# Kernel tuning notes

Measured on AMD Instinct MI355X. Metric: run time of the kernel, lower is better.

## Reference

```python
import jax, jax.numpy as jnp
import numpy as np

N = 50000      # nodes
E = 800000     # edges (avg degree 16)
F_IN = 32      # raw node feature dim
H = 96         # hidden_channels == encoder.output_dim (skip_connection=True)
EDGE_DIM = 16
L = 3          # num_layers
B = 50         # graphs in batch
MSG_IN = 2 * H + 1 + EDGE_DIM   # [h_i, h_j, ||dpos||^2, edge_attr]
NODE_IN = 2 * H                 # [h_i, aggregated message]


def setup_inputs() -> dict:
    key = jax.random.key(0)
    ks = jax.random.split(key, 14)

    def w(k, shape):
        fan_in = shape[-2]
        return jax.random.normal(k, shape, jnp.float32) * (1.0 / np.sqrt(fan_in))

    return {
        "x": jax.random.normal(ks[0], (N, F_IN), jnp.float32),
        "pos": jax.random.normal(ks[1], (N, 3), jnp.float32),
        "edge_index": jax.random.randint(ks[2], (2, E), 0, N),
        "edge_attr": jax.random.normal(ks[3], (E, EDGE_DIM), jnp.float32),
        "batch_indices": jnp.sort(jax.random.randint(ks[4], (N,), 0, B)),
        # encoder (modeled as a linear projection to H)
        "We": w(ks[5], (F_IN, H)), "be": jnp.zeros((H,), jnp.float32),
        # per-layer EGNN edge MLP: Linear(MSG_IN,H)-SiLU-Linear(H,H)-SiLU
        "eW1": w(ks[6], (L, MSG_IN, H)), "eb1": jnp.zeros((L, H), jnp.float32),
        "eW2": w(ks[7], (L, H, H)), "eb2": jnp.zeros((L, H), jnp.float32),
        # per-layer EGNN node MLP: Linear(NODE_IN,H)-SiLU-Linear(H,H)
        "nW1": w(ks[8], (L, NODE_IN, H)), "nb1": jnp.zeros((L, H), jnp.float32),
        "nW2": w(ks[9], (L, H, H)), "nb2": jnp.zeros((L, H), jnp.float32),
        "Wl": w(ks[10], (H, 1)), "bl": jnp.zeros((1,), jnp.float32),
    }


def reference(x, pos, edge_index, edge_attr, batch_indices,
              We, be, eW1, eb1, eW2, eb2, nW1, nb1, nW2, nb2, Wl, bl):
    silu = jax.nn.silu
    src, dst = edge_index[0], edge_index[1]

    # encoder: project raw features to hidden dim
    h = x @ We + be                                    # [N, H]

    # squared pairwise distances along edges (pos fixed, update_pos=False)
    rel = pos[src] - pos[dst]                          # [E, 3]
    d2 = jnp.sum(rel * rel, axis=-1, keepdims=True)    # [E, 1]

    for l in range(L):
        feat = jnp.concatenate([h[src], h[dst], d2, edge_attr], axis=-1)  # [E, MSG_IN]
        m = silu(silu(feat @ eW1[l] + eb1[l]) @ eW2[l] + eb2[l])          # [E, H]
        agg = jax.ops.segment_sum(m, dst, num_segments=N)                 # [N, H]
        upd = silu(jnp.concatenate([h, agg], axis=-1) @ nW1[l] + nb1[l]) @ nW2[l] + nb2[l]
        h = h + upd  # skip_connection=True

    # global_mean_pool over graphs
    counts = jax.ops.segment_sum(jnp.ones((N, 1), h.dtype), batch_indices, num_segments=B)
    pooled = jax.ops.segment_sum(h, batch_indices, num_segments=B) / jnp.maximum(counts, 1.0)

    return pooled @ Wl + bl                            # [B, 1]
```

## Files before the change

kernel.cpp:

```cpp
#include <hip/hip_runtime.h>

#define Nn 50000
#define Ee 800000
#define FIN 32
#define EDIM 16
#define Bb 50
#define SPX 6250

typedef _Float16 half8 __attribute__((ext_vector_type(8)));
typedef float floatx4 __attribute__((ext_vector_type(4)));

#define OFF_WeT 0
#define WT_LAYER(l) (3072 + (l) * 58368)
#define OFF_W1AB 0
#define OFF_W1C  18432
#define OFF_W2   21504
#define OFF_NW1  30720
#define OFF_NW2  49152
#define WT_TOTAL 178176

__device__ __forceinline__ float silu_f(float x) {
    return __fdividef(x, 1.0f + __expf(-x));
}

__device__ __forceinline__ int lower_bound_i(const int* a, int n, int v) {
    int lo = 0, hi = n;
    while (lo < hi) { int m = (lo + hi) >> 1; if (a[m] < v) lo = m + 1; else hi = m; }
    return lo;
}

__device__ __forceinline__ half8 ldg_h8(const _Float16* p) {
    return *(const half8*)p;
}

__device__ __forceinline__ half8 h8_zero() {
    half8 z;
    #pragma unroll
    for (int j = 0; j < 8; j++) z[j] = (_Float16)0.f;
    return z;
}

__global__ void k_prepw(const float* __restrict__ We, const float* __restrict__ eW1,
                        const float* __restrict__ eW2, const float* __restrict__ nW1,
                        const float* __restrict__ nW2, _Float16* __restrict__ wT) {
    int idx = blockIdx.x * 256 + threadIdx.x;
    if (idx >= WT_TOTAL) return;
    float v;
    if (idx < 3072) {
        int n = idx >> 5, k = idx & 31;
        v = We[k * 96 + n];
    } else {
        int j = idx - 3072;
        int l = j / 58368, r = j % 58368;
        const float* eW1l = eW1 + l * 209 * 96;
        if (r < 18432) {
            int n = r / 96, k = r % 96;
            v = (n < 96) ? eW1l[k * 96 + n] : eW1l[(96 + k) * 96 + (n - 96)];
        } else if (r < 21504) {
            int r2 = r - 18432;
            int n = r2 >> 5, k = r2 & 31;
            v = (k < 16) ? eW1l[(193 + k) * 96 + n]
              : (k == 16) ? eW1l[192 * 96 + n] : 0.f;
        } else if (r < 30720) {
            int r2 = r - 21504;
            int n = r2 / 96, k = r2 % 96;
            v = eW2[l * 9216 + k * 96 + n];
        } else if (r < 49152) {
            int r2 = r - 30720;
            int n = r2 / 192, k = r2 % 192;
            v = nW1[l * 18432 + k * 96 + n];
        } else {
            int r2 = r - 49152;
            int n = r2 / 96, k = r2 % 96;
            v = nW2[l * 9216 + k * 96 + n];
        }
    }
    wT[idx] = (_Float16)v;
}

__global__ void k_prep(const int* __restrict__ ei, int* __restrict__ counts) {
    int e = blockIdx.x * 256 + threadIdx.x;
    if (e >= Ee) return;
    atomicAdd(&counts[ei[Ee + e]], 1);
}

__global__ void k_scanA(const int* __restrict__ counts, int* __restrict__ rowstart,
                        int* __restrict__ bsums) {
    __shared__ int s[256];
    int b = blockIdx.x, t = threadIdx.x, i = b * 256 + t;
    int v = (i < Nn) ? counts[i] : 0;
    s[t] = v;
    __syncthreads();
    for (int off = 1; off < 256; off <<= 1) {
        int add = (t >= off) ? s[t - off] : 0;
        __syncthreads();
        s[t] += add;
        __syncthreads();
    }
    if (i < Nn) rowstart[i + 1] = s[t];
    if (t == 255) bsums[b] = s[255];
}

__global__ void k_scanB(int* __restrict__ bsums, int nb) {
    __shared__ int s[256];
    int t = threadIdx.x;
    int v = (t < nb) ? bsums[t] : 0;
    s[t] = v;
    __syncthreads();
    for (int off = 1; off < 256; off <<= 1) {
        int add = (t >= off) ? s[t - off] : 0;
        __syncthreads();
        s[t] += add;
        __syncthreads();
    }
    if (t < nb) bsums[t] = s[t] - v;
}

__global__ void k_scanC(int* __restrict__ rowstart, const int* __restrict__ bsums) {
    int b = blockIdx.x, t = threadIdx.x, i = b * 256 + t;
    if (i < Nn) rowstart[i + 1] += bsums[b];
    if (i == 0 && b == 0) rowstart[0] = 0;
}

__global__ void k_fill(const int* __restrict__ ei, const float* __restrict__ ea,
                       const float* __restrict__ pos, const int* __restrict__ rowstart,
                       int* __restrict__ cur, int* __restrict__ srcs_p,
                       int* __restrict__ dsts_p, _Float16* __restrict__ eap16,
                       _Float16* __restrict__ d2h) {
    int e = blockIdx.x * 256 + threadIdx.x;
    if (e >= Ee) return;
    int s = ei[e], d = ei[Ee + e];
    int slot = rowstart[d] + atomicAdd(&cur[d], 1);
    srcs_p[slot] = s;
    dsts_p[slot] = d;
    float dx = pos[s * 3 + 0] - pos[d * 3 + 0];
    float dy = pos[s * 3 + 1] - pos[d * 3 + 1];
    float dz = pos[s * 3 + 2] - pos[d * 3 + 2];
    float dv = dx * dx + dy * dy + dz * dz;
    const float4* ea4 = (const float4*)ea;
    float4 q0 = ea4[e * 4 + 0], q1 = ea4[e * 4 + 1];
    float4 q2 = ea4[e * 4 + 2], q3 = ea4[e * 4 + 3];
    half8 c0, c1;
    c0[0]=(_Float16)q0.x; c0[1]=(_Float16)q0.y; c0[2]=(_Float16)q0.z; c0[3]=(_Float16)q0.w;
    c0[4]=(_Float16)q1.x; c0[5]=(_Float16)q1.y; c0[6]=(_Float16)q1.z; c0[7]=(_Float16)q1.w;
    c1[0]=(_Float16)q2.x; c1[1]=(_Float16)q2.y; c1[2]=(_Float16)q2.z; c1[3]=(_Float16)q2.w;
    c1[4]=(_Float16)q3.x; c1[5]=(_Float16)q3.y; c1[6]=(_Float16)q3.z; c1[7]=(_Float16)q3.w;
    half8* dst8 = (half8*)(eap16 + (size_t)slot * 16);
    dst8[0] = c0; dst8[1] = c1;
    d2h[slot] = (_Float16)dv;
}

__global__ __launch_bounds__(256, 4)
void k_encab(const float* __restrict__ x, const _Float16* __restrict__ WeT,
             const float* __restrict__ be, const _Float16* __restrict__ W1abT,
             _Float16* __restrict__ h16, _Float16* __restrict__ A16,
             _Float16* __restrict__ B16, float* __restrict__ agg) {
    __shared__ _Float16 x16[64][40];
    __shared__ _Float16 hs[64][104];
    int t = threadIdx.x;
    int n0 = blockIdx.x * 64;
    for (int i = t; i < 64 * 32; i += 256) {
        int nl = i >> 5, k = i & 31;
        int n = n0 + nl;
        x16[nl][k] = (_Float16)((n < Nn) ? x[n * FIN + k] : 0.f);
    }
    __syncthreads();
    int lane = t & 63, quad = lane >> 4, lm = lane & 15, w = t >> 6;
    half8 af = *(const half8*)&x16[w * 16 + lm][quad * 8];
    #pragma unroll
    for (int nt = 0; nt < 6; nt++) {
        int col = nt * 16 + lm;
        float b = be[col];
        floatx4 acc = {b, b, b, b};
        half8 bf = ldg_h8(WeT + col * 32 + quad * 8);
        acc = __builtin_amdgcn_mfma_f32_16x16x32_f16(af, bf, acc, 0, 0, 0);
        #pragma unroll
        for (int r = 0; r < 4; r++)
            hs[w * 16 + quad * 4 + r][col] = (_Float16)acc[r];
    }
    __syncthreads();
    #pragma unroll
    for (int i = 0; i < 3; i++) {
        int ci = t + 256 * i;
        int el = ci / 12, c0 = (ci % 12) * 8;
        int n = n0 + el;
        if (n < Nn) *(half8*)(h16 + n * 96 + c0) = *(half8*)&hs[el][c0];
    }
    for (int i = t; i < 64 * 24; i += 256) {
        int el = i / 24, c = (i % 24) * 4;
        int n = n0 + el;
        if (n < Nn) *(float4*)(agg + n * 96 + c) = make_float4(0.f, 0.f, 0.f, 0.f);
    }
    half8 af3[3];
    #pragma unroll
    for (int kt = 0; kt < 3; kt++)
        af3[kt] = *(const half8*)&hs[w * 16 + lm][kt * 32 + quad * 8];
    #pragma unroll
    for (int nt = 0; nt < 12; nt++) {
        int col = nt * 16 + lm;
        floatx4 acc = {0.f, 0.f, 0.f, 0.f};
        #pragma unroll
        for (int kt = 0; kt < 3; kt++) {
            half8 bf = ldg_h8(W1abT + col * 96 + kt * 32 + quad * 8);
            acc = __builtin_amdgcn_mfma_f32_16x16x32_f16(af3[kt], bf, acc, 0, 0, 0);
        }
        #pragma unroll
        for (int r = 0; r < 4; r++) {
            int n = n0 + w * 16 + quad * 4 + r;
            if (n < Nn) {
                if (col < 96) A16[n * 96 + col] = (_Float16)acc[r];
                else          B16[n * 96 + col - 96] = (_Float16)acc[r];
            }
        }
    }
}

__global__ __launch_bounds__(256, 4)
void k_edge(const _Float16* __restrict__ A16, const _Float16* __restrict__ B16,
            const _Float16* __restrict__ eap16, const _Float16* __restrict__ d2h,
            const int* __restrict__ srcs_p, const int* __restrict__ dsts_p,
            const _Float16* __restrict__ W1cT, const float* __restrict__ eb1l,
            const _Float16* __restrict__ W2T, const float* __restrict__ eb2l,
            float* __restrict__ agg) {
    __shared__ _Float16 u16[64][104];
    __shared__ _Float16 W2f[18 * 64 * 8];
    __shared__ _Float16 W1f[6 * 64 * 8];
    __shared__ int ss_s[4][16], ds_s[4][16];

    int t = threadIdx.x;
    int lane = t & 63, quad = lane >> 4, lm = lane & 15, w = t >> 6;

    for (int f = w; f < 18; f += 4) {
        int nt = f / 3, kt = f % 3;
        half8 v = ldg_h8(W2T + (nt * 16 + lm) * 96 + kt * 32 + quad * 8);
        *(half8*)&W2f[(f * 64 + lane) * 8] = v;
    }
    for (int f = w; f < 6; f += 4) {
        half8 v = ldg_h8(W1cT + (f * 16 + lm) * 32 + quad * 8);
        *(half8*)&W1f[(f * 64 + lane) * 8] = v;
    }
    float eb1v[6], eb2v[6];
    #pragma unroll
    for (int nt = 0; nt < 6; nt++) {
        eb1v[nt] = eb1l[nt * 16 + lm];
        eb2v[nt] = eb2l[nt * 16 + lm];
    }
    __syncthreads();

    int xcd = blockIdx.x & 7, ib = blockIdx.x >> 3;
    int slot = ib * 4 + w;
    for (int s = slot; s < SPX; s += 512) {
        int e0 = (xcd * SPX + s) * 16;
        half8 af1;
        if (quad == 0)      af1 = ldg_h8(eap16 + (size_t)(e0 + lm) * 16);
        else if (quad == 1) af1 = ldg_h8(eap16 + (size_t)(e0 + lm) * 16 + 8);
        else { af1 = h8_zero(); if (quad == 2) af1[0] = d2h[e0 + lm]; }
        if (lane < 16) {
            ss_s[w][lane] = srcs_p[e0 + lane];
            ds_s[w][lane] = dsts_p[e0 + lane];
        }
        #pragma unroll
        for (int nt = 0; nt < 6; nt++) {
            floatx4 acc = {eb1v[nt], eb1v[nt], eb1v[nt], eb1v[nt]};
            half8 bf = *(const half8*)&W1f[(nt * 64 + lane) * 8];
            acc = __builtin_amdgcn_mfma_f32_16x16x32_f16(af1, bf, acc, 0, 0, 0);
            #pragma unroll
            for (int r = 0; r < 4; r++)
                u16[w * 16 + quad * 4 + r][nt * 16 + lm] = (_Float16)acc[r];
        }
        #pragma unroll
        for (int i = 0; i < 3; i++) {
            int ci = lane + 64 * i;
            int el = ci / 12, c0 = (ci % 12) * 8;
            half8 av = ldg_h8(A16 + ss_s[w][el] * 96 + c0);
            half8 bv = ldg_h8(B16 + ds_s[w][el] * 96 + c0);
            half8 pv = *(half8*)&u16[w * 16 + el][c0];
            half8 sum = pv + av + bv;
            half8 res;
            #pragma unroll
            for (int j = 0; j < 8; j++)
                res[j] = (_Float16)silu_f((float)sum[j]);
            *(half8*)&u16[w * 16 + el][c0] = res;
        }
        half8 af2[3];
        #pragma unroll
        for (int kt = 0; kt < 3; kt++)
            af2[kt] = *(const half8*)&u16[w * 16 + lm][kt * 32 + quad * 8];
        #pragma unroll
        for (int nt = 0; nt < 6; nt++) {
            floatx4 acc = {eb2v[nt], eb2v[nt], eb2v[nt], eb2v[nt]};
            #pragma unroll
            for (int kt = 0; kt < 3; kt++) {
                half8 bf = *(const half8*)&W2f[((nt * 3 + kt) * 64 + lane) * 8];
                acc = __builtin_amdgcn_mfma_f32_16x16x32_f16(af2[kt], bf, acc, 0, 0, 0);
            }
            #pragma unroll
            for (int r = 0; r < 4; r++)
                u16[w * 16 + quad * 4 + r][nt * 16 + lm] = (_Float16)silu_f(acc[r]);
        }
        if (lane < 48) {
            int c = lane * 2;
            float run0 = 0.f, run1 = 0.f;
            int cd = ds_s[w][0];
            #pragma unroll
            for (int e = 0; e < 16; e++) {
                int dn = ds_s[w][e];
                if (dn != cd) {
                    atomicAdd(&agg[cd * 96 + c], run0);
                    atomicAdd(&agg[cd * 96 + c + 1], run1);
                    run0 = 0.f; run1 = 0.f; cd = dn;
                }
                _Float16 v0 = u16[w * 16 + e][c];
                _Float16 v1 = u16[w * 16 + e][c + 1];
                run0 += (float)v0;
                run1 += (float)v1;
            }
            atomicAdd(&agg[cd * 96 + c], run0);
            atomicAdd(&agg[cd * 96 + c + 1], run1);
        }
    }
}

__global__ __launch_bounds__(256, 4)
void k_nodeab(_Float16* __restrict__ h16, float* __restrict__ agg,
              const _Float16* __restrict__ nW1T, const float* __restrict__ nb1l,
              const _Float16* __restrict__ nW2T, const float* __restrict__ nb2l,
              const _Float16* __restrict__ W1abT, _Float16* __restrict__ A16,
              _Float16* __restrict__ B16, int do_ab) {
    __shared__ _Float16 in16[64][200];
    __shared__ _Float16 t116[64][104];
    int t = threadIdx.x, n0 = blockIdx.x * 64;
    #pragma unroll
    for (int i = 0; i < 3; i++) {
        int ci = t + 256 * i;
        int el = ci / 12, c0 = (ci % 12) * 8;
        int n = n0 + el;
        half8 hv = h8_zero();
        half8 av = h8_zero();
        if (n < Nn) {
            hv = ldg_h8(h16 + n * 96 + c0);
            float4 a = *(const float4*)(agg + n * 96 + c0);
            float4 b = *(const float4*)(agg + n * 96 + c0 + 4);
            av[0]=(_Float16)a.x; av[1]=(_Float16)a.y; av[2]=(_Float16)a.z; av[3]=(_Float16)a.w;
            av[4]=(_Float16)b.x; av[5]=(_Float16)b.y; av[6]=(_Float16)b.z; av[7]=(_Float16)b.w;
        }
        *(half8*)&in16[el][c0] = hv;
        *(half8*)&in16[el][96 + c0] = av;
    }
    __syncthreads();
    int lane = t & 63, quad = lane >> 4, lm = lane & 15, w = t >> 6;
    half8 af[6];
    #pragma unroll
    for (int kt = 0; kt < 6; kt++)
        af[kt] = *(const half8*)&in16[w * 16 + lm][kt * 32 + quad * 8];
    #pragma unroll
    for (int nt = 0; nt < 6; nt++) {
        int col = nt * 16 + lm;
        float b = nb1l[col];
        floatx4 acc = {b, b, b, b};
        #pragma unroll
        for (int kt = 0; kt < 6; kt++) {
            half8 bf = ldg_h8(nW1T + col * 192 + kt * 32 + quad * 8);
            acc = __builtin_amdgcn_mfma_f32_16x16x32_f16(af[kt], bf, acc, 0, 0, 0);
        }
        #pragma unroll
        for (int r = 0; r < 4; r++)
            t116[w * 16 + quad * 4 + r][col] = (_Float16)silu_f(acc[r]);
    }
    half8 af2[3];
    #pragma unroll
    for (int kt = 0; kt < 3; kt++)
        af2[kt] = *(const half8*)&t116[w * 16 + lm][kt * 32 + quad * 8];
    #pragma unroll
    for (int nt = 0; nt < 6; nt++) {
        int col = nt * 16 + lm;
        float b = nb2l[col];
        floatx4 acc = {b, b, b, b};
        #pragma unroll
        for (int kt = 0; kt < 3; kt++) {
            half8 bf = ldg_h8(nW2T + col * 96 + kt * 32 + quad * 8);
            acc = __builtin_amdgcn_mfma_f32_16x16x32_f16(af2[kt], bf, acc, 0, 0, 0);
        }
        #pragma unroll
        for (int r = 0; r < 4; r++) {
            int row = w * 16 + quad * 4 + r;
            float hnew = (float)in16[row][col] + acc[r];
            in16[row][col] = (_Float16)hnew;
        }
    }
    __syncthreads();
    #pragma unroll
    for (int i = 0; i < 3; i++) {
        int ci = t + 256 * i;
        int el = ci / 12, c0 = (ci % 12) * 8;
        int n = n0 + el;
        if (n < Nn) *(half8*)(h16 + n * 96 + c0) = *(half8*)&in16[el][c0];
    }
    if (!do_ab) return;
    half8 af3[3];
    #pragma unroll
    for (int kt = 0; kt < 3; kt++)
        af3[kt] = *(const half8*)&in16[w * 16 + lm][kt * 32 + quad * 8];
    #pragma unroll
    for (int nt = 0; nt < 12; nt++) {
        int col = nt * 16 + lm;
        floatx4 acc = {0.f, 0.f, 0.f, 0.f};
        #pragma unroll
        for (int kt = 0; kt < 3; kt++) {
            half8 bf = ldg_h8(W1abT + col * 96 + kt * 32 + quad * 8);
            acc = __builtin_amdgcn_mfma_f32_16x16x32_f16(af3[kt], bf, acc, 0, 0, 0);
        }
        #pragma unroll
        for (int r = 0; r < 4; r++) {
            int n = n0 + w * 16 + quad * 4 + r;
            if (n < Nn) {
                if (col < 96) A16[n * 96 + col] = (_Float16)acc[r];
                else          B16[n * 96 + col - 96] = (_Float16)acc[r];
            }
        }
    }
    for (int i = t; i < 64 * 24; i += 256) {
        int el = i / 24, c = (i % 24) * 4;
        int n = n0 + el;
        if (n < Nn) *(float4*)(agg + n * 96 + c) = make_float4(0.f, 0.f, 0.f, 0.f);
    }
}

__global__ void k_pool_partial(const _Float16* __restrict__ h16, const int* __restrict__ batch,
                               float* __restrict__ pooled) {
    int g = blockIdx.x >> 2, q = blockIdx.x & 3;
    int start = lower_bound_i(batch, Nn, g);
    int end   = lower_bound_i(batch, Nn, g + 1);
    int len = end - start;
    int chunk = (len + 3) >> 2;
    int s = start + q * chunk;
    int e = min(s + chunk, end);
    int t = threadIdx.x;
    int j = t % 96, r = t / 96;
    float sum = 0.f;
    for (int n = s + r; n < e; n += 2) sum += (float)h16[n * 96 + j];
    atomicAdd(&pooled[g * 96 + j], sum);
}

__global__ void k_final(const float* __restrict__ pooled, const int* __restrict__ batch,
                        const float* __restrict__ Wl, const float* __restrict__ bl,
                        float* __restrict__ out) {
    int g = blockIdx.x, lane = threadIdx.x;
    int start = lower_bound_i(batch, Nn, g);
    int end   = lower_bound_i(batch, Nn, g + 1);
    int cnt = end - start; if (cnt < 1) cnt = 1;
    float v = 0.f;
    for (int j = lane; j < 96; j += 64) v += pooled[g * 96 + j] * Wl[j];
    #pragma unroll
    for (int off = 32; off > 0; off >>= 1) v += __shfl_down(v, off);
    if (lane == 0) out[g] = v / (float)cnt + bl[0];
}

extern "C" void kernel_launch(void* const* d_in, const int* in_sizes, int n_in,
                              void* d_out, int out_size, void* d_ws, size_t ws_size,
                              hipStream_t stream) {
    const float* x     = (const float*)d_in[0];
    const float* pos   = (const float*)d_in[1];
    const int*   ei    = (const int*)d_in[2];
    const float* ea    = (const float*)d_in[3];
    const int*   batch = (const int*)d_in[4];
    const float* We    = (const float*)d_in[5];
    const float* be    = (const float*)d_in[6];
    const float* eW1   = (const float*)d_in[7];
    const float* eb1   = (const float*)d_in[8];
    const float* eW2   = (const float*)d_in[9];
    const float* eb2   = (const float*)d_in[10];
    const float* nW1   = (const float*)d_in[11];
    const float* nb1   = (const float*)d_in[12];
    const float* nW2   = (const float*)d_in[13];
    const float* nb2   = (const float*)d_in[14];
    const float* Wl    = (const float*)d_in[15];
    const float* bl    = (const float*)d_in[16];
    float* out = (float*)d_out;

    float* ws = (float*)d_ws;
    _Float16* h16    = (_Float16*)(ws);
    _Float16* A16    = (_Float16*)(ws + 2400000);
    _Float16* B16    = (_Float16*)(ws + 4800000);
    float*    agg    = ws + 7200000;
    float*    pooled = ws + 12000000;
    int*      counts   = (int*)(ws + 12004800);
    int*      cur      = (int*)(ws + 12054800);
    int*      rowstart = (int*)(ws + 12104800);
    int*      bsums    = (int*)(ws + 12154816);
    int*      srcs_p   = (int*)(ws + 12155072);
    int*      dsts_p   = (int*)(ws + 12955072);
    _Float16* eap16    = (_Float16*)(ws + 13755072);
    _Float16* d2h      = (_Float16*)(ws + 20155072);
    _Float16* wT       = (_Float16*)(ws + 20555072);

    hipMemsetAsync(counts, 0, 2 * 50000 * sizeof(int), stream);
    hipMemsetAsync(pooled, 0, Bb * 96 * sizeof(float), stream);

    k_prepw<<<dim3(696), dim3(256), 0, stream>>>(We, eW1, eW2, nW1, nW2, wT);
    k_prep<<<dim3(3125), dim3(256), 0, stream>>>(ei, counts);
    k_scanA<<<dim3(196), dim3(256), 0, stream>>>(counts, rowstart, bsums);
    k_scanB<<<dim3(1), dim3(256), 0, stream>>>(bsums, 196);
    k_scanC<<<dim3(196), dim3(256), 0, stream>>>(rowstart, bsums);
    k_fill<<<dim3(3125), dim3(256), 0, stream>>>(ei, ea, pos, rowstart, cur,
                                                 srcs_p, dsts_p, eap16, d2h);
    k_encab<<<dim3(782), dim3(256), 0, stream>>>(x, wT + OFF_WeT, be,
        wT + WT_LAYER(0) + OFF_W1AB, h16, A16, B16, agg);

    for (int l = 0; l < 3; l++) {
        const _Float16* wl = wT + WT_LAYER(l);
        k_edge<<<dim3(1024), dim3(256), 0, stream>>>(A16, B16, eap16, d2h,
            srcs_p, dsts_p, wl + OFF_W1C, eb1 + l * 96, wl + OFF_W2, eb2 + l * 96, agg);
        const _Float16* wnext = wT + WT_LAYER(l < 2 ? l + 1 : 0);
        k_nodeab<<<dim3(782), dim3(256), 0, stream>>>(h16, agg,
            wl + OFF_NW1, nb1 + l * 96, wl + OFF_NW2, nb2 + l * 96,
            wnext + OFF_W1AB, A16, B16, (l < 2) ? 1 : 0);
    }
    k_pool_partial<<<dim3(200), dim3(192), 0, stream>>>(h16, batch, pooled);
    k_final<<<dim3(50), dim3(64), 0, stream>>>(pooled, batch, Wl, bl, out);
}
```

Measured before the change: 761.4 us.

## Fuse mean-pool into last node kernel and widen edge scatter to per-column lanes

In the last layer the node-update kernel now sums its 64 updated rows per graph straight from shared memory and adds them atomically into pooled. This removes the separate pooling kernel, the final h16 store and its re-read. The edge kernel's segmented scatter now gives each lane a single column (96 lanes in two passes) instead of column pairs on 48 lanes. That spreads the atomics over more lanes but adds a second pass per wave. The fused pool issues up to a few atomics per block per column into a small pooled array shared by 782 blocks, which may contend.

New measurement: 738.5 us. 1.03x faster.

```diff
diff --git a/kernel.cpp b/kernel.cpp
--- a/kernel.cpp
+++ b/kernel.cpp
@@ -298,25 +298,20 @@
             for (int r = 0; r < 4; r++)
                 u16[w * 16 + quad * 4 + r][nt * 16 + lm] = (_Float16)silu_f(acc[r]);
         }
-        if (lane < 48) {
-            int c = lane * 2;
-            float run0 = 0.f, run1 = 0.f;
-            int cd = ds_s[w][0];
-            #pragma unroll
-            for (int e = 0; e < 16; e++) {
-                int dn = ds_s[w][e];
-                if (dn != cd) {
-                    atomicAdd(&agg[cd * 96 + c], run0);
-                    atomicAdd(&agg[cd * 96 + c + 1], run1);
-                    run0 = 0.f; run1 = 0.f; cd = dn;
+        #pragma unroll
+        for (int p = 0; p < 2; p++) {
+            int c = lane + p * 64;
+            if (c < 96) {
+                float run = 0.f;
+                int cd = ds_s[w][0];
+                #pragma unroll
+                for (int e = 0; e < 16; e++) {
+                    int dn = ds_s[w][e];
+                    if (dn != cd) { atomicAdd(&agg[cd * 96 + c], run); run = 0.f; cd = dn; }
+                    run += (float)u16[w * 16 + e][c];
                 }
-                _Float16 v0 = u16[w * 16 + e][c];
-                _Float16 v1 = u16[w * 16 + e][c + 1];
-                run0 += (float)v0;
-                run1 += (float)v1;
+                atomicAdd(&agg[cd * 96 + c], run);
             }
-            atomicAdd(&agg[cd * 96 + c], run0);
-            atomicAdd(&agg[cd * 96 + c + 1], run1);
         }
     }
 }
@@ -326,9 +321,11 @@
               const _Float16* __restrict__ nW1T, const float* __restrict__ nb1l,
               const _Float16* __restrict__ nW2T, const float* __restrict__ nb2l,
               const _Float16* __restrict__ W1abT, _Float16* __restrict__ A16,
-              _Float16* __restrict__ B16, int do_ab) {
+              _Float16* __restrict__ B16, const int* __restrict__ batch,
+              float* __restrict__ pooled, int do_ab) {
     __shared__ _Float16 in16[64][200];
     __shared__ _Float16 t116[64][104];
+    __shared__ int gb_s[64];
     int t = threadIdx.x, n0 = blockIdx.x * 64;
     #pragma unroll
     for (int i = 0; i < 3; i++) {
@@ -347,6 +344,10 @@
         *(half8*)&in16[el][c0] = hv;
         *(half8*)&in16[el][96 + c0] = av;
     }
+    if (!do_ab && t < 64) {
+        int n = n0 + t;
+        gb_s[t] = (n < Nn) ? batch[n] : -1;
+    }
     __syncthreads();
     int lane = t & 63, quad = lane >> 4, lm = lane & 15, w = t >> 6;
     half8 af[6];
@@ -389,6 +390,22 @@
         }
     }
     __syncthreads();
+    if (!do_ab) {
+        if (t < 96) {
+            float run = 0.f;
+            int cd = gb_s[0];
+            for (int e = 0; e < 64; e++) {
+                int g = gb_s[e];
+                if (g != cd) {
+                    if (cd >= 0) atomicAdd(&pooled[cd * 96 + t], run);
+                    run = 0.f; cd = g;
+                }
+                run += (float)in16[e][t];
+            }
+            if (cd >= 0) atomicAdd(&pooled[cd * 96 + t], run);
+        }
+        return;
+    }
     #pragma unroll
     for (int i = 0; i < 3; i++) {
         int ci = t + 256 * i;
@@ -396,7 +413,6 @@
         int n = n0 + el;
         if (n < Nn) *(half8*)(h16 + n * 96 + c0) = *(half8*)&in16[el][c0];
     }
-    if (!do_ab) return;
     half8 af3[3];
     #pragma unroll
     for (int kt = 0; kt < 3; kt++)
@@ -424,22 +440,6 @@
         int n = n0 + el;
         if (n < Nn) *(float4*)(agg + n * 96 + c) = make_float4(0.f, 0.f, 0.f, 0.f);
     }
-}
-
-__global__ void k_pool_partial(const _Float16* __restrict__ h16, const int* __restrict__ batch,
-                               float* __restrict__ pooled) {
-    int g = blockIdx.x >> 2, q = blockIdx.x & 3;
-    int start = lower_bound_i(batch, Nn, g);
-    int end   = lower_bound_i(batch, Nn, g + 1);
-    int len = end - start;
-    int chunk = (len + 3) >> 2;
-    int s = start + q * chunk;
-    int e = min(s + chunk, end);
-    int t = threadIdx.x;
-    int j = t % 96, r = t / 96;
-    float sum = 0.f;
-    for (int n = s + r; n < e; n += 2) sum += (float)h16[n * 96 + j];
-    atomicAdd(&pooled[g * 96 + j], sum);
 }
 
 __global__ void k_final(const float* __restrict__ pooled, const int* __restrict__ batch,
@@ -514,8 +514,7 @@
         const _Float16* wnext = wT + WT_LAYER(l < 2 ? l + 1 : 0);
         k_nodeab<<<dim3(782), dim3(256), 0, stream>>>(h16, agg,
             wl + OFF_NW1, nb1 + l * 96, wl + OFF_NW2, nb2 + l * 96,
-            wnext + OFF_W1AB, A16, B16, (l < 2) ? 1 : 0);
-    }
-    k_pool_partial<<<dim3(200), dim3(192), 0, stream>>>(h16, batch, pooled);
+            wnext + OFF_W1AB, A16, B16, batch, pooled, (l < 2) ? 1 : 0);
+    }
     k_final<<<dim3(50), dim3(64), 0, stream>>>(pooled, batch, Wl, bl, out);
 }
```
